# Kernel tuning notes

Hardware: AMD Instinct MI355X
Metric: run time of the kernel (lower is better)

Reference implementation:

```python
import jax, jax.numpy as jnp
import numpy as np

D = 768        # embed_dim
P = 16         # patch_size
DEPTH = 12
FF = 3072      # dim_feedforward = 4*D
NUM_CLASSES = 100
EPS = 1e-5     # nn.LayerNorm default


def _ln(x, g, b):
    m = jnp.mean(x, axis=-1, keepdims=True)
    v = jnp.mean((x - m) ** 2, axis=-1, keepdims=True)
    return (x - m) / jnp.sqrt(v + EPS) * g + b


def setup_inputs() -> dict:
    key = jax.random.key(0)
    ks = jax.random.split(key, 24)
    f32 = jnp.float32
    inp = {
        'x': jax.random.normal(ks[0], (32, 3, 224, 224), dtype=f32),
        # patch embed conv: [C_in, P, P, D] layout for einsum
        'patch_w': jax.random.normal(ks[1], (3, P, P, D), dtype=f32) * 0.02,
        'patch_b': jnp.zeros((D,), f32),
        'cls_token': jax.random.normal(ks[2], (1, 1, D), dtype=f32) * 0.02,
        'pos_embed': jax.random.normal(ks[3], (1, 197, D), dtype=f32) * 0.02,
        # stacked per-layer params; Linear stored as [in, out]
        'Wq': jax.random.normal(ks[4], (DEPTH, D, D), dtype=f32) * 0.02,
        'bq': jnp.zeros((DEPTH, D), f32),
        'Wk': jax.random.normal(ks[5], (DEPTH, D, D), dtype=f32) * 0.02,
        'bk': jnp.zeros((DEPTH, D), f32),
        'Wv': jax.random.normal(ks[6], (DEPTH, D, D), dtype=f32) * 0.02,
        'bv': jnp.zeros((DEPTH, D), f32),
        'W1': jax.random.normal(ks[7], (DEPTH, D, FF), dtype=f32) * 0.02,
        'b1': jnp.zeros((DEPTH, FF), f32),
        'W2': jax.random.normal(ks[8], (DEPTH, FF, D), dtype=f32) * 0.02,
        'b2': jnp.zeros((DEPTH, D), f32),
        'ln1_g': jnp.ones((DEPTH, D), f32),
        'ln1_b': jnp.zeros((DEPTH, D), f32),
        'ln2_g': jnp.ones((DEPTH, D), f32),
        'ln2_b': jnp.zeros((DEPTH, D), f32),
        'lnf_g': jnp.ones((D,), f32),
        'lnf_b': jnp.zeros((D,), f32),
        'head_w': jax.random.normal(ks[9], (D, NUM_CLASSES), dtype=f32) * 0.02,
        'head_b': jnp.zeros((NUM_CLASSES,), f32),
    }
    return inp


def reference(x, patch_w, patch_b, cls_token, pos_embed,
              Wq, bq, Wk, bk, Wv, bv, W1, b1, W2, b2,
              ln1_g, ln1_b, ln2_g, ln2_b, lnf_g, lnf_b,
              head_w, head_b):
    B = x.shape[0]
    Hp = x.shape[2] // P  # 14
    # patch embed: Conv2d(k=16, s=16) == non-overlapping patch projection
    xp = x.reshape(B, 3, Hp, P, Hp, P)
    tok = jnp.einsum('bchpwq,cpqd->bhwd', xp, patch_w).reshape(B, Hp * Hp, D) + patch_b
    tok = jnp.concatenate([jnp.broadcast_to(cls_token, (B, 1, D)), tok], axis=1)
    tok = tok + pos_embed  # [B, 197, D]
    N = tok.shape[1]
    # gumbel noise for F.gumbel_softmax(tau=1, hard=False), one sample per layer
    gnoise = jax.random.gumbel(jax.random.key(1), (DEPTH, B, N, N), dtype=tok.dtype)
    inv_sqrt_d = 1.0 / jnp.sqrt(jnp.asarray(D, tok.dtype))

    def step(src, p):
        (wq, bq_, wk, bk_, wv, bv_, w1, b1_, w2, b2_,
         g1, be1, g2, be2, gn) = p
        Q = src @ wq + bq_
        K = src @ wk + bk_
        V = src @ wv + bv_
        scores = jnp.einsum('bnd,bmd->bnm', Q, K) * inv_sqrt_d
        attn = jax.nn.softmax(scores + gn, axis=-1) @ V
        src = _ln(src + attn, g1, be1)          # note: out_linear unused in source
        ff = jax.nn.gelu(src @ w1 + b1_, approximate=False) @ w2 + b2_
        src = _ln(src + ff, g2, be2)
        return src, None

    xs = (Wq, bq, Wk, bk, Wv, bv, W1, b1, W2, b2,
          ln1_g, ln1_b, ln2_g, ln2_b, gnoise)
    tok, _ = jax.lax.scan(step, tok, xs)
    tok = _ln(tok, lnf_g, lnf_b)
    cls = tok[:, 0]
    return cls @ head_w + head_b
```

## Files before the change

### kernel.cpp

```cpp
#include <hip/hip_runtime.h>
#include <hip/hip_bf16.h>
#include <math.h>


namespace {
constexpr int DIM    = 768;
constexpr int FF_DIM = 3072;
constexpr int QKVN   = 2304;
constexpr int NTOK   = 197;
constexpr int NBATCH = 32;
constexpr int NLAYER = 12;
constexpr int ROWS   = NBATCH * NTOK;
constexpr int NPATCH = 196;
constexpr int PROWS  = NBATCH * NPATCH;
constexpr int KVPAD  = 256;
constexpr float LN_EPS = 1e-5f;
}

typedef __attribute__((ext_vector_type(8))) __bf16 bf16x8;
typedef __attribute__((ext_vector_type(4))) float  f32x4;

__device__ __forceinline__ unsigned rotl32(unsigned v, int d) {
  return (v << d) | (v >> (32 - d));
}

__device__ __forceinline__ float gumbel_noise(unsigned idx) {
  const unsigned ks0 = 0u, ks1 = 1u, ks2 = 0x1BD11BDBu;
  unsigned x0 = 0u + ks0;
  unsigned x1 = idx + ks1;
#define TFR(r) { x0 += x1; x1 = rotl32(x1, (r)); x1 ^= x0; }
  TFR(13) TFR(15) TFR(26) TFR(6)   x0 += ks1; x1 += ks2 + 1u;
  TFR(17) TFR(29) TFR(16) TFR(24)  x0 += ks2; x1 += ks0 + 2u;
  TFR(13) TFR(15) TFR(26) TFR(6)   x0 += ks0; x1 += ks1 + 3u;
  TFR(17) TFR(29) TFR(16) TFR(24)  x0 += ks1; x1 += ks2 + 4u;
  TFR(13) TFR(15) TFR(26) TFR(6)   x0 += ks2; x1 += ks0 + 5u;
#undef TFR
  unsigned bits = x0 ^ x1;
  float f = __uint_as_float((bits >> 9) | 0x3f800000u) - 1.0f;
  const float tiny = 1.17549435e-38f;
  float u = fmaxf(tiny, f + tiny);
  return -logf(-logf(u));
}

__device__ __forceinline__ float block_reduce_sum(float val, float* red) {
  int tid = threadIdx.x;
  red[tid] = val; __syncthreads();
  for (int off = 128; off > 0; off >>= 1) {
    if (tid < off) red[tid] += red[tid + off];
    __syncthreads();
  }
  float r = red[0];
  __syncthreads();
  return r;
}

__device__ __forceinline__ float block_reduce_max(float val, float* red) {
  int tid = threadIdx.x;
  red[tid] = val; __syncthreads();
  for (int off = 128; off > 0; off >>= 1) {
    if (tid < off) red[tid] = fmaxf(red[tid], red[tid + off]);
    __syncthreads();
  }
  float r = red[0];
  __syncthreads();
  return r;
}

__device__ __forceinline__ void async_copy16(const void* g, void* l) {
  __builtin_amdgcn_global_load_lds(
      (const __attribute__((address_space(1))) unsigned*)g,
      (__attribute__((address_space(3))) unsigned*)l, 16, 0, 0);
}

__device__ __forceinline__ int xcd_swizzle(int id, int nwg) {
  const int q = nwg >> 3, r = nwg & 7;
  const int xcd = id & 7, pos = id >> 3;
  return (xcd < r ? xcd * (q + 1) : r * (q + 1) + (xcd - r) * q) + pos;
}

template<int STORE, bool GELU>
__global__ void mm_nt(
    const __hip_bfloat16* __restrict__ A, long sA, int lda,
    const __hip_bfloat16* __restrict__ B, long sB, int ldb,
    void* __restrict__ Cv, long sC, int ldc,
    int M, int N, int K, const float* __restrict__ bias) {
  __shared__ __hip_bfloat16 As[128 * 64];
  __shared__ __hip_bfloat16 Bs[128 * 64];
  const int bz = blockIdx.y;
  A += (long)bz * sA;
  B += (long)bz * sB;
  const int tilesN = (N + 127) >> 7;
  const int id = xcd_swizzle(blockIdx.x, gridDim.x);
  const int row0 = (id / tilesN) * 128, col0 = (id % tilesN) * 128;

  const int tid = threadIdx.x, lane = tid & 63, wid = tid >> 6;
  const int wr = (wid >> 1) * 64, wc = (wid & 1) * 64;
  const int fr = lane & 15;
  const int kh = lane >> 4;
  const int fsw = fr & 7;
  f32x4 acc[4][4] = {};

  const int elem = wid * 512 + lane * 8;

  for (int k0 = 0; k0 < K; k0 += 64) {
    #pragma unroll
    for (int c = 0; c < 4; c++) {
      const int e = c * 2048 + elem;
      const int r = e >> 6;
      const int slot = (e >> 3) & 7;
      const int ksw = ((slot ^ (r & 7)) << 3);
      async_copy16(A + (long)(row0 + r) * lda + k0 + ksw,
                   (char*)As + c * 4096 + wid * 1024);
    }
    #pragma unroll
    for (int c = 0; c < 4; c++) {
      const int e = c * 2048 + elem;
      const int r = e >> 6;
      const int slot = (e >> 3) & 7;
      const int ksw = ((slot ^ (r & 7)) << 3);
      async_copy16(B + (long)(col0 + r) * ldb + k0 + ksw,
                   (char*)Bs + c * 4096 + wid * 1024);
    }
    __syncthreads();
    #pragma unroll
    for (int ks = 0; ks < 2; ks++) {
      bf16x8 a[4], b[4];
      #pragma unroll
      for (int i = 0; i < 4; i++) {
        const int row = wr + i * 16 + fr;
        const int sl  = ((ks << 2) | kh) ^ fsw;
        a[i] = *(const bf16x8*)((const char*)As + row * 128 + (sl << 4));
      }
      #pragma unroll
      for (int j = 0; j < 4; j++) {
        const int row = wc + j * 16 + fr;
        const int sl  = ((ks << 2) | kh) ^ fsw;
        b[j] = *(const bf16x8*)((const char*)Bs + row * 128 + (sl << 4));
      }
      #pragma unroll
      for (int i = 0; i < 4; i++)
        #pragma unroll
        for (int j = 0; j < 4; j++)
          acc[i][j] = __builtin_amdgcn_mfma_f32_16x16x32_bf16(
              a[i], b[j], acc[i][j], 0, 0, 0);
    }
    __syncthreads();
  }

  #pragma unroll
  for (int i = 0; i < 4; i++) {
    #pragma unroll
    for (int j = 0; j < 4; j++) {
      #pragma unroll
      for (int t = 0; t < 4; t++) {
        const int r  = row0 + wr + i * 16 + kh * 4 + t;
        const int cc = col0 + wc + j * 16 + fr;
        if (r < M && cc < N) {
          float v = acc[i][j][t];
          if (bias) v += bias[cc];
          if (GELU) v = 0.5f * v * (1.0f + erff(v * 0.70710678118654752f));
          if (STORE == 0)
            ((float*)Cv)[(long)bz * sC + (long)r * ldc + cc] = v;
          else
            ((__hip_bfloat16*)Cv)[(long)bz * sC + (long)r * ldc + cc] =
                __float2bfloat16(v);
        }
      }
    }
  }
}

__global__ void transpose_bf16_kernel(const float* __restrict__ W,
                                      __hip_bfloat16* __restrict__ Wt,
                                      int K, int N) {
  __shared__ float t[32][33];
  const int k0 = blockIdx.x * 32, n0 = blockIdx.y * 32;
  const int tx = threadIdx.x & 31, ty = threadIdx.x >> 5;
  #pragma unroll
  for (int i = 0; i < 32; i += 8)
    t[ty + i][tx] = W[(long)(k0 + ty + i) * N + n0 + tx];
  __syncthreads();
  #pragma unroll
  for (int i = 0; i < 32; i += 8)
    Wt[(long)(n0 + ty + i) * K + k0 + tx] = __float2bfloat16(t[tx][ty + i]);
}

__global__ void wtrans_layer(const float* __restrict__ Wq,
                             const float* __restrict__ Wk,
                             const float* __restrict__ Wv,
                             const float* __restrict__ W1,
                             const float* __restrict__ W2,
                             __hip_bfloat16* __restrict__ wqkv_t,
                             __hip_bfloat16* __restrict__ w1_t,
                             __hip_bfloat16* __restrict__ w2_t) {
  __shared__ float t[32][33];
  const int id = blockIdx.x;
  const float* W; __hip_bfloat16* O; int K, N, k0, n0;
  if (id < 1728) {
    const int m = id / 576, tt = id % 576;
    W = (m == 0) ? Wq : (m == 1) ? Wk : Wv;
    O = wqkv_t + (long)m * DIM * DIM;
    K = DIM; N = DIM; k0 = (tt / 24) * 32; n0 = (tt % 24) * 32;
  } else if (id < 4032) {
    const int tt = id - 1728;
    W = W1; O = w1_t;
    K = DIM; N = FF_DIM; k0 = (tt / 96) * 32; n0 = (tt % 96) * 32;
  } else {
    const int tt = id - 4032;
    W = W2; O = w2_t;
    K = FF_DIM; N = DIM; k0 = (tt / 24) * 32; n0 = (tt % 24) * 32;
  }
  const int tx = threadIdx.x & 31, ty = threadIdx.x >> 5;
  #pragma unroll
  for (int i = 0; i < 32; i += 8)
    t[ty + i][tx] = W[(long)(k0 + ty + i) * N + n0 + tx];
  __syncthreads();
  #pragma unroll
  for (int i = 0; i < 32; i += 8)
    O[(long)(n0 + ty + i) * K + k0 + tx] = __float2bfloat16(t[tx][ty + i]);
}

__global__ void build_qkv_bias(const float* __restrict__ bq,
                               const float* __restrict__ bk,
                               const float* __restrict__ bv,
                               float* __restrict__ o) {
  const int l = blockIdx.x;
  for (int d = threadIdx.x; d < DIM; d += 256) {
    o[l * QKVN + d]           = bq[l * DIM + d];
    o[l * QKVN + DIM + d]     = bk[l * DIM + d];
    o[l * QKVN + 2 * DIM + d] = bv[l * DIM + d];
  }
}

__global__ void vtrans_kernel(const __hip_bfloat16* __restrict__ qkv,
                              __hip_bfloat16* __restrict__ vt) {
  __shared__ __hip_bfloat16 s[64][68];
  const int b = blockIdx.z;
  const int t0 = blockIdx.x * 64;
  const int d0 = blockIdx.y * 64;
  const int tx = threadIdx.x & 63, ty = threadIdx.x >> 6;
  for (int i = ty; i < 64; i += 4) {
    const int t = t0 + i;
    __hip_bfloat16 v = __float2bfloat16(0.f);
    if (t < NTOK) v = qkv[(long)(b * NTOK + t) * QKVN + 2 * DIM + d0 + tx];
    s[i][tx] = v;
  }
  __syncthreads();
  for (int i = ty; i < 64; i += 4)
    vt[((long)b * DIM + d0 + i) * KVPAD + t0 + tx] = s[tx][i];
}

__global__ void im2col_kernel(const float* __restrict__ x,
                              __hip_bfloat16* __restrict__ col) {
  const int p = blockIdx.x;
  const int b = p / NPATCH, pi = p % NPATCH;
  const int h = pi / 14, w = pi % 14;
  for (int e = threadIdx.x; e < DIM; e += 256) {
    const int c = e >> 8, r = e & 255, pp = r >> 4, q = r & 15;
    col[(long)p * DIM + e] = __float2bfloat16(
        x[(((long)b * 3 + c) * 224 + h * 16 + pp) * 224 + w * 16 + q]);
  }
}

__global__ void assemble_kernel(const float* __restrict__ tmp,
                                const float* __restrict__ cls,
                                const float* __restrict__ pos,
                                float* __restrict__ tok,
                                __hip_bfloat16* __restrict__ tok_bf) {
  const int row = blockIdx.x;
  const int b = row / NTOK, n = row % NTOK;
  for (int d = threadIdx.x; d < DIM; d += 256) {
    float v = (n == 0) ? cls[d] : tmp[(long)(b * NPATCH + n - 1) * DIM + d];
    v += pos[n * DIM + d];
    tok[(long)row * DIM + d] = v;
    tok_bf[(long)row * DIM + d] = __float2bfloat16(v);
  }
}

__global__ void softmax_kernel(const float* __restrict__ sc,
                               __hip_bfloat16* __restrict__ P, int layer) {
  __shared__ float red[256];
  const int row = blockIdx.x;
  const int b = row / NTOK, n = row % NTOK;
  const int tid = threadIdx.x;
  const long base = (long)row * NTOK;
  const float inv_sqrt_d = 0.036084391824351615f;

  float x = -INFINITY;
  if (tid < NTOK) {
    const unsigned idx =
        ((((unsigned)layer * NBATCH + b) * NTOK + n) * NTOK) + tid;
    x = sc[base + tid] * inv_sqrt_d + gumbel_noise(idx);
  }
  const float mx = block_reduce_max(x, red);
  float ex = (tid < NTOK) ? expf(x - mx) : 0.f;
  const float s = block_reduce_sum(ex, red);
  const float pv = (tid < NTOK) ? ex / s : 0.f;
  P[(long)row * KVPAD + tid] = __float2bfloat16(pv);
}

__global__ void add_ln_kernel(float* __restrict__ tok,
                              __hip_bfloat16* __restrict__ tok_bf,
                              const float* __restrict__ res,
                              const float* __restrict__ g,
                              const float* __restrict__ beta) {
  __shared__ float red[256];
  const int row = blockIdx.x;
  const int tid = threadIdx.x;
  const long base = (long)row * DIM;
  float v[3];
  float s = 0.f;
  #pragma unroll
  for (int i = 0; i < 3; i++) {
    const int d = tid + (i << 8);
    v[i] = tok[base + d] + res[base + d];
    s += v[i];
  }
  const float mean = block_reduce_sum(s, red) * (1.0f / DIM);
  float s2 = 0.f;
  #pragma unroll
  for (int i = 0; i < 3; i++) { const float dd = v[i] - mean; s2 += dd * dd; }
  const float var = block_reduce_sum(s2, red) * (1.0f / DIM);
  const float inv = 1.0f / sqrtf(var + LN_EPS);
  #pragma unroll
  for (int i = 0; i < 3; i++) {
    const int d = tid + (i << 8);
    const float o = (v[i] - mean) * inv * g[d] + beta[d];
    tok[base + d] = o;
    tok_bf[base + d] = __float2bfloat16(o);
  }
}

__global__ void head_kernel(const float* __restrict__ tok,
                            const float* __restrict__ g,
                            const float* __restrict__ beta,
                            const float* __restrict__ hw,
                            const float* __restrict__ hb,
                            float* __restrict__ out) {
  __shared__ float red[256];
  __shared__ float xn[DIM];
  const int b = blockIdx.x;
  const int tid = threadIdx.x;
  const float* xr = tok + (long)b * NTOK * DIM;
  float v[3];
  float s = 0.f;
  #pragma unroll
  for (int i = 0; i < 3; i++) { v[i] = xr[tid + (i << 8)]; s += v[i]; }
  const float mean = block_reduce_sum(s, red) * (1.0f / DIM);
  float s2 = 0.f;
  #pragma unroll
  for (int i = 0; i < 3; i++) { const float dd = v[i] - mean; s2 += dd * dd; }
  const float var = block_reduce_sum(s2, red) * (1.0f / DIM);
  const float inv = 1.0f / sqrtf(var + LN_EPS);
  #pragma unroll
  for (int i = 0; i < 3; i++) {
    const int d = tid + (i << 8);
    xn[d] = (v[i] - mean) * inv * g[d] + beta[d];
  }
  __syncthreads();
  for (int c = tid; c < 100; c += 256) {
    float acc = hb[c];
    for (int d = 0; d < DIM; d++) acc += xn[d] * hw[d * 100 + c];
    out[b * 100 + c] = acc;
  }
}

extern "C" void kernel_launch(void* const* d_in, const int* in_sizes, int n_in,
                              void* d_out, int out_size, void* d_ws, size_t ws_size,
                              hipStream_t stream) {
  const float* x        = (const float*)d_in[0];
  const float* patch_w  = (const float*)d_in[1];
  const float* patch_b  = (const float*)d_in[2];
  const float* cls_tok  = (const float*)d_in[3];
  const float* pos_emb  = (const float*)d_in[4];
  const float* Wq       = (const float*)d_in[5];
  const float* bq       = (const float*)d_in[6];
  const float* Wk       = (const float*)d_in[7];
  const float* bk       = (const float*)d_in[8];
  const float* Wv       = (const float*)d_in[9];
  const float* bv       = (const float*)d_in[10];
  const float* W1       = (const float*)d_in[11];
  const float* b1       = (const float*)d_in[12];
  const float* W2       = (const float*)d_in[13];
  const float* b2       = (const float*)d_in[14];
  const float* ln1_g    = (const float*)d_in[15];
  const float* ln1_b    = (const float*)d_in[16];
  const float* ln2_g    = (const float*)d_in[17];
  const float* ln2_b    = (const float*)d_in[18];
  const float* lnf_g    = (const float*)d_in[19];
  const float* lnf_b    = (const float*)d_in[20];
  const float* head_w   = (const float*)d_in[21];
  const float* head_b   = (const float*)d_in[22];
  float* out = (float*)d_out;

  float* fb = (float*)d_ws;
  long fo = 0;
  float* tok      = fb + fo; fo += 6400L * DIM;
  float* b4       = fb + fo; fo += 6400L * DIM;
  float* scbuf    = fb + fo; fo += 1241920L;
  float* bias_all = fb + fo; fo += (long)NLAYER * QKVN;
  __hip_bfloat16* hbuf = (__hip_bfloat16*)(fb + fo);
  long ho = 0;
  __hip_bfloat16* tok_bf = hbuf + ho; ho += 6400L * DIM;
  __hip_bfloat16* qkv    = hbuf + ho;
  __hip_bfloat16* ffout  = hbuf + ho; ho += 6400L * FF_DIM;
  __hip_bfloat16* vt     = hbuf + ho; ho += (long)NBATCH * DIM * KVPAD;
  __hip_bfloat16* Pb     = hbuf + ho; ho += 6400L * KVPAD;
  __hip_bfloat16* wqkv_t = hbuf + ho; ho += (long)QKVN * DIM;
  __hip_bfloat16* w1_t   = hbuf + ho; ho += (long)FF_DIM * DIM;
  __hip_bfloat16* w2_t   = hbuf + ho; ho += (long)DIM * FF_DIM;

  const long DD = (long)DIM * DIM;
  const long QKVSTRIDE = (long)NTOK * QKVN;
  const long TOKSTRIDE = (long)NTOK * DIM;
  const long SCSTRIDE  = (long)NTOK * NTOK;
  const long VTSTRIDE  = (long)DIM * KVPAD;
  const long PSTRIDE   = (long)NTOK * KVPAD;

  build_qkv_bias<<<NLAYER, 256, 0, stream>>>(bq, bk, bv, bias_all);

  im2col_kernel<<<PROWS, 256, 0, stream>>>(x, ffout);
  transpose_bf16_kernel<<<dim3(DIM / 32, DIM / 32), 256, 0, stream>>>(
      patch_w, wqkv_t, DIM, DIM);
  mm_nt<0, false><<<dim3(49 * 6, 1), 256, 0, stream>>>(
      ffout, 0, DIM, wqkv_t, 0, DIM, b4, 0, DIM, PROWS, DIM, DIM, patch_b);
  assemble_kernel<<<ROWS, 256, 0, stream>>>(b4, cls_tok, pos_emb, tok, tok_bf);

  for (int l = 0; l < NLAYER; l++) {
    wtrans_layer<<<6336, 256, 0, stream>>>(
        Wq + l * DD, Wk + l * DD, Wv + l * DD,
        W1 + (long)l * DIM * FF_DIM, W2 + (long)l * FF_DIM * DIM,
        wqkv_t, w1_t, w2_t);

    mm_nt<1, false><<<dim3(50 * (QKVN / 128), 1), 256, 0, stream>>>(
        tok_bf, 0, DIM, wqkv_t, 0, DIM, qkv, 0, QKVN,
        ROWS, QKVN, DIM, bias_all + l * QKVN);

    vtrans_kernel<<<dim3(KVPAD / 64, DIM / 64, NBATCH), 256, 0, stream>>>(qkv, vt);

    mm_nt<0, false><<<dim3(2 * 2, NBATCH), 256, 0, stream>>>(
        qkv, QKVSTRIDE, QKVN, qkv + DIM, QKVSTRIDE, QKVN, scbuf, SCSTRIDE, NTOK,
        NTOK, NTOK, DIM, nullptr);

    softmax_kernel<<<ROWS, 256, 0, stream>>>(scbuf, Pb, l);

    mm_nt<0, false><<<dim3(2 * (DIM / 128), NBATCH), 256, 0, stream>>>(
        Pb, PSTRIDE, KVPAD, vt, VTSTRIDE, KVPAD, b4, TOKSTRIDE, DIM,
        NTOK, DIM, KVPAD, nullptr);

    add_ln_kernel<<<ROWS, 256, 0, stream>>>(tok, tok_bf, b4,
        ln1_g + l * DIM, ln1_b + l * DIM);

    mm_nt<1, true><<<dim3(50 * (FF_DIM / 128), 1), 256, 0, stream>>>(
        tok_bf, 0, DIM, w1_t, 0, DIM, ffout, 0, FF_DIM,
        ROWS, FF_DIM, DIM, b1 + l * FF_DIM);
    mm_nt<0, false><<<dim3(50 * (DIM / 128), 1), 256, 0, stream>>>(
        ffout, 0, FF_DIM, w2_t, 0, FF_DIM, b4, 0, DIM,
        ROWS, DIM, FF_DIM, b2 + l * DIM);

    add_ln_kernel<<<ROWS, 256, 0, stream>>>(tok, tok_bf, b4,
        ln2_g + l * DIM, ln2_b + l * DIM);
  }

  head_kernel<<<NBATCH, 256, 0, stream>>>(tok, lnf_g, lnf_b, head_w, head_b, out);
}
```

Measured before the change: 3.003 ms.

## Double-buffer GEMM LDS tiles to overlap async global loads with MFMA

The bf16 GEMM kernel now keeps two LDS buffers for the A and B tiles. It prefetches two K-tiles ahead with async global-to-LDS copies, and it replaces the full __syncthreads with an explicit vmcnt wait plus s_barrier. The goal is to hide global-load latency behind MFMA work instead of stalling on every K step. In exchange, LDS use per block doubles to 64KB, which can lower occupancy. Correctness also now depends on the hand-counted vmcnt(8) matching exactly the eight outstanding copies per stage.

```diff
diff --git a/kernel.cpp b/kernel.cpp
--- a/kernel.cpp
+++ b/kernel.cpp
@@ -84,8 +84,8 @@
     const __hip_bfloat16* __restrict__ B, long sB, int ldb,
     void* __restrict__ Cv, long sC, int ldc,
     int M, int N, int K, const float* __restrict__ bias) {
-  __shared__ __hip_bfloat16 As[128 * 64];
-  __shared__ __hip_bfloat16 Bs[128 * 64];
+  __shared__ __hip_bfloat16 As[2][128 * 64];
+  __shared__ __hip_bfloat16 Bs[2][128 * 64];
   const int bz = blockIdx.y;
   A += (long)bz * sA;
   B += (long)bz * sB;
@@ -102,7 +102,7 @@
 
   const int elem = wid * 512 + lane * 8;
 
-  for (int k0 = 0; k0 < K; k0 += 64) {
+  auto stage = [&](int buf, int k0) {
     #pragma unroll
     for (int c = 0; c < 4; c++) {
       const int e = c * 2048 + elem;
@@ -110,18 +110,20 @@
       const int slot = (e >> 3) & 7;
       const int ksw = ((slot ^ (r & 7)) << 3);
       async_copy16(A + (long)(row0 + r) * lda + k0 + ksw,
-                   (char*)As + c * 4096 + wid * 1024);
+                   (char*)&As[buf][0] + c * 4096 + wid * 1024);
+      async_copy16(B + (long)(col0 + r) * ldb + k0 + ksw,
+                   (char*)&Bs[buf][0] + c * 4096 + wid * 1024);
     }
-    #pragma unroll
-    for (int c = 0; c < 4; c++) {
-      const int e = c * 2048 + elem;
-      const int r = e >> 6;
-      const int slot = (e >> 3) & 7;
-      const int ksw = ((slot ^ (r & 7)) << 3);
-      async_copy16(B + (long)(col0 + r) * ldb + k0 + ksw,
-                   (char*)Bs + c * 4096 + wid * 1024);
-    }
-    __syncthreads();
+  };
+
+  const int nt = K >> 6;
+  stage(0, 0);
+  if (nt > 1) stage(1, 64);
+  int cur = 0;
+  for (int t = 0; t < nt; ++t) {
+    if (t + 1 < nt) asm volatile("s_waitcnt vmcnt(8)" ::: "memory");
+    else            asm volatile("s_waitcnt vmcnt(0)" ::: "memory");
+    __builtin_amdgcn_s_barrier();
     #pragma unroll
     for (int ks = 0; ks < 2; ks++) {
       bf16x8 a[4], b[4];
@@ -129,13 +131,13 @@
       for (int i = 0; i < 4; i++) {
         const int row = wr + i * 16 + fr;
         const int sl  = ((ks << 2) | kh) ^ fsw;
-        a[i] = *(const bf16x8*)((const char*)As + row * 128 + (sl << 4));
+        a[i] = *(const bf16x8*)((const char*)&As[cur][0] + row * 128 + (sl << 4));
       }
       #pragma unroll
       for (int j = 0; j < 4; j++) {
         const int row = wc + j * 16 + fr;
         const int sl  = ((ks << 2) | kh) ^ fsw;
-        b[j] = *(const bf16x8*)((const char*)Bs + row * 128 + (sl << 4));
+        b[j] = *(const bf16x8*)((const char*)&Bs[cur][0] + row * 128 + (sl << 4));
       }
       #pragma unroll
       for (int i = 0; i < 4; i++)
@@ -144,7 +146,9 @@
           acc[i][j] = __builtin_amdgcn_mfma_f32_16x16x32_bf16(
               a[i], b[j], acc[i][j], 0, 0, 0);
     }
-    __syncthreads();
+    __builtin_amdgcn_s_barrier();
+    if (t + 2 < nt) stage(cur, (t + 2) << 6);
+    cur ^= 1;
   }
 
   #pragma unroll
```

New measurement: 3.342 ms. +11.3%, slower.

## Hoist weight transposes out of layer loop and split-K the FF2 GEMM

Applied to the files above, without the earlier changes.

All twelve layers' weights are transposed to bf16 in one launch before the layer loop, using 64x64 tiles, when the workspace is large enough. The per-layer transpose launch runs only as a fallback. The FF2 GEMM is split along K into two halves written to separate buffers, and the second layer norm sums both partials plus the bias. The split targets the low block count of the N=768 GEMM, at the cost of an extra partial-buffer read in add_ln. The score buffer is moved to alias space after qkv, which enlarges the workspace requirement.

```diff
diff --git a/kernel.cpp b/kernel.cpp
--- a/kernel.cpp
+++ b/kernel.cpp
@@ -185,39 +185,50 @@
     Wt[(long)(n0 + ty + i) * K + k0 + tx] = __float2bfloat16(t[tx][ty + i]);
 }
 
-__global__ void wtrans_layer(const float* __restrict__ Wq,
-                             const float* __restrict__ Wk,
-                             const float* __restrict__ Wv,
-                             const float* __restrict__ W1,
-                             const float* __restrict__ W2,
-                             __hip_bfloat16* __restrict__ wqkv_t,
-                             __hip_bfloat16* __restrict__ w1_t,
-                             __hip_bfloat16* __restrict__ w2_t) {
-  __shared__ float t[32][33];
+__global__ void wtrans_kernel(const float* __restrict__ Wq,
+                              const float* __restrict__ Wk,
+                              const float* __restrict__ Wv,
+                              const float* __restrict__ W1,
+                              const float* __restrict__ W2,
+                              __hip_bfloat16* __restrict__ wqkv_t,
+                              __hip_bfloat16* __restrict__ w1_t,
+                              __hip_bfloat16* __restrict__ w2_t,
+                              long sq, long s1, long s2) {
+  __shared__ float t[64][65];
+  const int l = blockIdx.y;
+  Wq += (long)l * DIM * DIM;  Wk += (long)l * DIM * DIM;
+  Wv += (long)l * DIM * DIM;
+  W1 += (long)l * DIM * FF_DIM;  W2 += (long)l * FF_DIM * DIM;
+  wqkv_t += (long)l * sq;  w1_t += (long)l * s1;  w2_t += (long)l * s2;
+
   const int id = blockIdx.x;
   const float* W; __hip_bfloat16* O; int K, N, k0, n0;
-  if (id < 1728) {
-    const int m = id / 576, tt = id % 576;
+  if (id < 432) {
+    const int m = id / 144, tt = id % 144;
     W = (m == 0) ? Wq : (m == 1) ? Wk : Wv;
     O = wqkv_t + (long)m * DIM * DIM;
-    K = DIM; N = DIM; k0 = (tt / 24) * 32; n0 = (tt % 24) * 32;
-  } else if (id < 4032) {
-    const int tt = id - 1728;
+    K = DIM; N = DIM; k0 = (tt / 12) * 64; n0 = (tt % 12) * 64;
+  } else if (id < 1008) {
+    const int tt = id - 432;
     W = W1; O = w1_t;
-    K = DIM; N = FF_DIM; k0 = (tt / 96) * 32; n0 = (tt % 96) * 32;
+    K = DIM; N = FF_DIM; k0 = (tt / 48) * 64; n0 = (tt % 48) * 64;
   } else {
-    const int tt = id - 4032;
+    const int tt = id - 1008;
     W = W2; O = w2_t;
-    K = FF_DIM; N = DIM; k0 = (tt / 24) * 32; n0 = (tt % 24) * 32;
-  }
-  const int tx = threadIdx.x & 31, ty = threadIdx.x >> 5;
-  #pragma unroll
-  for (int i = 0; i < 32; i += 8)
-    t[ty + i][tx] = W[(long)(k0 + ty + i) * N + n0 + tx];
+    K = FF_DIM; N = DIM; k0 = (tt / 12) * 64; n0 = (tt % 12) * 64;
+  }
+  const int tx = threadIdx.x & 63, ty = threadIdx.x >> 6;
+  #pragma unroll
+  for (int i = 0; i < 16; i++) {
+    const int r = ty + i * 4;
+    t[r][tx] = W[(long)(k0 + r) * N + n0 + tx];
+  }
   __syncthreads();
   #pragma unroll
-  for (int i = 0; i < 32; i += 8)
-    O[(long)(n0 + ty + i) * K + k0 + tx] = __float2bfloat16(t[tx][ty + i]);
+  for (int i = 0; i < 16; i++) {
+    const int r = ty + i * 4;
+    O[(long)(n0 + r) * K + k0 + tx] = __float2bfloat16(t[tx][r]);
+  }
 }
 
 __global__ void build_qkv_bias(const float* __restrict__ bq,
@@ -302,6 +313,8 @@
 __global__ void add_ln_kernel(float* __restrict__ tok,
                               __hip_bfloat16* __restrict__ tok_bf,
                               const float* __restrict__ res,
+                              const float* __restrict__ res2,
+                              const float* __restrict__ rbias,
                               const float* __restrict__ g,
                               const float* __restrict__ beta) {
   __shared__ float red[256];
@@ -313,8 +326,11 @@
   #pragma unroll
   for (int i = 0; i < 3; i++) {
     const int d = tid + (i << 8);
-    v[i] = tok[base + d] + res[base + d];
-    s += v[i];
+    float r = tok[base + d] + res[base + d];
+    if (res2)  r += res2[base + d];
+    if (rbias) r += rbias[d];
+    v[i] = r;
+    s += r;
   }
   const float mean = block_reduce_sum(s, red) * (1.0f / DIM);
   float s2 = 0.f;
@@ -393,22 +409,37 @@
   const float* head_b   = (const float*)d_in[22];
   float* out = (float*)d_out;
 
+  const long WQKV = (long)QKVN * DIM;
+  const long W1SZ = (long)FF_DIM * DIM;
+  const long W2SZ = (long)DIM * FF_DIM;
+  const long WLAYER = WQKV + W1SZ + W2SZ;
+
+  const long F32N = 3L * 6400 * DIM + (long)NLAYER * QKVN;
+  const long BF16FIX = 6400L * DIM + 6400L * FF_DIM +
+                       (long)NBATCH * DIM * KVPAD + 6400L * KVPAD +
+                       (long)DIM * DIM;
+  const size_t need12 = (size_t)F32N * 4 + (size_t)(BF16FIX + 12 * WLAYER) * 2;
+  const bool hoist = ws_size >= need12;
+  const int NW = hoist ? NLAYER : 1;
+
   float* fb = (float*)d_ws;
   long fo = 0;
   float* tok      = fb + fo; fo += 6400L * DIM;
   float* b4       = fb + fo; fo += 6400L * DIM;
-  float* scbuf    = fb + fo; fo += 1241920L;
+  float* b4b      = fb + fo; fo += 6400L * DIM;
   float* bias_all = fb + fo; fo += (long)NLAYER * QKVN;
   __hip_bfloat16* hbuf = (__hip_bfloat16*)(fb + fo);
   long ho = 0;
   __hip_bfloat16* tok_bf = hbuf + ho; ho += 6400L * DIM;
   __hip_bfloat16* qkv    = hbuf + ho;
   __hip_bfloat16* ffout  = hbuf + ho; ho += 6400L * FF_DIM;
+  float* scbuf = (float*)(qkv + 6400L * QKVN);
   __hip_bfloat16* vt     = hbuf + ho; ho += (long)NBATCH * DIM * KVPAD;
   __hip_bfloat16* Pb     = hbuf + ho; ho += 6400L * KVPAD;
-  __hip_bfloat16* wqkv_t = hbuf + ho; ho += (long)QKVN * DIM;
-  __hip_bfloat16* w1_t   = hbuf + ho; ho += (long)FF_DIM * DIM;
-  __hip_bfloat16* w2_t   = hbuf + ho; ho += (long)DIM * FF_DIM;
+  __hip_bfloat16* pw_t   = hbuf + ho; ho += (long)DIM * DIM;
+  __hip_bfloat16* wqkv_t = hbuf + ho; ho += (long)NW * WQKV;
+  __hip_bfloat16* w1_t   = hbuf + ho; ho += (long)NW * W1SZ;
+  __hip_bfloat16* w2_t   = hbuf + ho; ho += (long)NW * W2SZ;
 
   const long DD = (long)DIM * DIM;
   const long QKVSTRIDE = (long)NTOK * QKVN;
@@ -419,21 +450,31 @@
 
   build_qkv_bias<<<NLAYER, 256, 0, stream>>>(bq, bk, bv, bias_all);
 
+  if (hoist) {
+    wtrans_kernel<<<dim3(1584, NLAYER), 256, 0, stream>>>(
+        Wq, Wk, Wv, W1, W2, wqkv_t, w1_t, w2_t, WQKV, W1SZ, W2SZ);
+  }
+
   im2col_kernel<<<PROWS, 256, 0, stream>>>(x, ffout);
   transpose_bf16_kernel<<<dim3(DIM / 32, DIM / 32), 256, 0, stream>>>(
-      patch_w, wqkv_t, DIM, DIM);
+      patch_w, pw_t, DIM, DIM);
   mm_nt<0, false><<<dim3(49 * 6, 1), 256, 0, stream>>>(
-      ffout, 0, DIM, wqkv_t, 0, DIM, b4, 0, DIM, PROWS, DIM, DIM, patch_b);
+      ffout, 0, DIM, pw_t, 0, DIM, b4, 0, DIM, PROWS, DIM, DIM, patch_b);
   assemble_kernel<<<ROWS, 256, 0, stream>>>(b4, cls_tok, pos_emb, tok, tok_bf);
 
   for (int l = 0; l < NLAYER; l++) {
-    wtrans_layer<<<6336, 256, 0, stream>>>(
-        Wq + l * DD, Wk + l * DD, Wv + l * DD,
-        W1 + (long)l * DIM * FF_DIM, W2 + (long)l * FF_DIM * DIM,
-        wqkv_t, w1_t, w2_t);
+    __hip_bfloat16* wqkv_l = wqkv_t + (hoist ? (long)l * WQKV : 0);
+    __hip_bfloat16* w1_l   = w1_t   + (hoist ? (long)l * W1SZ : 0);
+    __hip_bfloat16* w2_l   = w2_t   + (hoist ? (long)l * W2SZ : 0);
+    if (!hoist) {
+      wtrans_kernel<<<dim3(1584, 1), 256, 0, stream>>>(
+          Wq + l * DD, Wk + l * DD, Wv + l * DD,
+          W1 + (long)l * DIM * FF_DIM, W2 + (long)l * FF_DIM * DIM,
+          wqkv_l, w1_l, w2_l, 0, 0, 0);
+    }
 
     mm_nt<1, false><<<dim3(50 * (QKVN / 128), 1), 256, 0, stream>>>(
-        tok_bf, 0, DIM, wqkv_t, 0, DIM, qkv, 0, QKVN,
+        tok_bf, 0, DIM, wqkv_l, 0, DIM, qkv, 0, QKVN,
         ROWS, QKVN, DIM, bias_all + l * QKVN);
 
     vtrans_kernel<<<dim3(KVPAD / 64, DIM / 64, NBATCH), 256, 0, stream>>>(qkv, vt);
@@ -448,17 +489,18 @@
         Pb, PSTRIDE, KVPAD, vt, VTSTRIDE, KVPAD, b4, TOKSTRIDE, DIM,
         NTOK, DIM, KVPAD, nullptr);
 
-    add_ln_kernel<<<ROWS, 256, 0, stream>>>(tok, tok_bf, b4,
+    add_ln_kernel<<<ROWS, 256, 0, stream>>>(tok, tok_bf, b4, nullptr, nullptr,
         ln1_g + l * DIM, ln1_b + l * DIM);
 
     mm_nt<1, true><<<dim3(50 * (FF_DIM / 128), 1), 256, 0, stream>>>(
-        tok_bf, 0, DIM, w1_t, 0, DIM, ffout, 0, FF_DIM,
+        tok_bf, 0, DIM, w1_l, 0, DIM, ffout, 0, FF_DIM,
         ROWS, FF_DIM, DIM, b1 + l * FF_DIM);
-    mm_nt<0, false><<<dim3(50 * (DIM / 128), 1), 256, 0, stream>>>(
-        ffout, 0, FF_DIM, w2_t, 0, FF_DIM, b4, 0, DIM,
-        ROWS, DIM, FF_DIM, b2 + l * DIM);
-
-    add_ln_kernel<<<ROWS, 256, 0, stream>>>(tok, tok_bf, b4,
+
+    mm_nt<0, false><<<dim3(50 * (DIM / 128), 2), 256, 0, stream>>>(
+        ffout, 1536, FF_DIM, w2_l, 1536, FF_DIM,
+        b4, 6400L * DIM, DIM, ROWS, DIM, 1536, nullptr);
+
+    add_ln_kernel<<<ROWS, 256, 0, stream>>>(tok, tok_bf, b4, b4b, b2 + l * DIM,
         ln2_g + l * DIM, ln2_b + l * DIM);
   }
 
```

New measurement: 2.956 ms. No clear change (-1.6%).
